# Kernel tuning notes

Hardware: AMD Instinct MI355X
Metric: run time of the kernel (lower is better)

## Reference

```python
import jax, jax.numpy as jnp
import numpy as np

N_HEAD = 16
HEAD_DIM = 64
N_EMBD = N_HEAD * HEAD_DIM  # 1024


def setup_inputs() -> dict:
    key = jax.random.key(0)
    ks = jax.random.split(key, 5)
    B, S = 2, 2048
    x = jax.random.normal(ks[0], (B, S, N_EMBD), dtype=jnp.float32)
    qkv_w = jax.random.normal(ks[1], (N_EMBD, 3 * N_EMBD), dtype=jnp.float32) * 0.02
    qkv_b = jax.random.normal(ks[2], (3 * N_EMBD,), dtype=jnp.float32) * 0.02
    proj_w = jax.random.normal(ks[3], (N_EMBD, N_EMBD), dtype=jnp.float32) * 0.02
    proj_b = jax.random.normal(ks[4], (N_EMBD,), dtype=jnp.float32) * 0.02
    return {"x": x, "qkv_w": qkv_w, "qkv_b": qkv_b, "proj_w": proj_w, "proj_b": proj_b}


def reference(x, qkv_w, qkv_b, proj_w, proj_b):
    B, S, _ = x.shape
    qkv = x @ qkv_w + qkv_b  # [B,S,3E]
    q, k, v = jnp.split(qkv, 3, axis=-1)
    # [B,H,S,D]
    q = q.reshape(B, S, N_HEAD, HEAD_DIM).transpose(0, 2, 1, 3)
    k = k.reshape(B, S, N_HEAD, HEAD_DIM).transpose(0, 2, 1, 3)
    v = v.reshape(B, S, N_HEAD, HEAD_DIM).transpose(0, 2, 1, 3)
    scale = 1.0 / jnp.sqrt(jnp.float32(HEAD_DIM))
    scores = jnp.einsum('bhqd,bhkd->bhqk', q, k) * scale  # [B,H,S,S]
    causal = jnp.tril(jnp.ones((S, S), dtype=bool))
    scores = jnp.where(causal[None, None], scores, jnp.float32(-jnp.inf))
    attn = jax.nn.softmax(scores, axis=-1)  # dropout p=0 (eval)
    out = jnp.einsum('bhqk,bhkd->bhqd', attn, v)
    out = out.transpose(0, 2, 1, 3).reshape(B, S, N_EMBD)
    out = out @ proj_w + proj_b  # resid dropout p=0
    return out, k, v
```

## Files before the change

### kernel.cpp

```cpp
#include <hip/hip_runtime.h>
#include <hip/hip_bf16.h>


typedef __attribute__((ext_vector_type(4))) float f32x4;
typedef __attribute__((ext_vector_type(16))) float f32x16;
typedef __attribute__((ext_vector_type(8))) short s16x8;
typedef __attribute__((ext_vector_type(4))) short s16x4;

__device__ __forceinline__ short f2bf(float f) {
    union { float f; unsigned u; } x{f};
    unsigned r = x.u + 0x7fff + ((x.u >> 16) & 1);
    return (short)(r >> 16);
}

__device__ __forceinline__ void gload_lds16(const void* g, void* l) {
    __builtin_amdgcn_global_load_lds(
        (const __attribute__((address_space(1))) void*)g,
        (__attribute__((address_space(3))) void*)l, 16, 0, 0);
}

__global__ __launch_bounds__(256) void fused_prepass(const float* __restrict__ x,
                                                     short* __restrict__ x_bf,
                                                     const float* __restrict__ qkv_w,
                                                     short* __restrict__ wT1,
                                                     const float* __restrict__ proj_w,
                                                     short* __restrict__ wT2) {
    __shared__ float tile[32][33];
    const int bid = blockIdx.x, tid = threadIdx.x;
    if (bid < 2048) {
        int i = (bid * 256 + tid) * 8;
        f32x4 a = *(const f32x4*)&x[i];
        f32x4 b = *(const f32x4*)&x[i + 4];
        s16x8 o;
        #pragma unroll
        for (int j = 0; j < 4; ++j) o[j] = f2bf(a[j]);
        #pragma unroll
        for (int j = 0; j < 4; ++j) o[j + 4] = f2bf(b[j]);
        *(s16x8*)&x_bf[i] = o;
        return;
    }
    const float* in;
    short* out;
    int K = 1024, N, n0, k0;
    if (bid < 5120) {
        int blk = bid - 2048;
        in = qkv_w; out = wT1; N = 3072;
        n0 = (blk % 96) * 32; k0 = (blk / 96) * 32;
    } else {
        int blk = bid - 5120;
        in = proj_w; out = wT2; N = 1024;
        n0 = (blk & 31) * 32; k0 = (blk >> 5) * 32;
    }
    const int tx = tid & 31, ty = tid >> 5;
    #pragma unroll
    for (int r = 0; r < 4; ++r)
        tile[ty + r * 8][tx] = in[(long)(k0 + ty + r * 8) * N + n0 + tx];
    __syncthreads();
    #pragma unroll
    for (int r = 0; r < 4; ++r)
        out[(long)(n0 + ty + r * 8) * K + k0 + tx] = f2bf(tile[tx][ty + r * 8]);
}


template <int MODE>
__global__ __launch_bounds__(256) void gemm_bf16(
    const short* __restrict__ A, const short* __restrict__ Bt,
    const float* __restrict__ bias, int M, int N, int K,
    float* __restrict__ outf,
    short* __restrict__ qbf, short* __restrict__ kbf, short* __restrict__ vbfT,
    float* __restrict__ kout, float* __restrict__ vout) {
    __shared__ __align__(16) short As[128 * 32];
    __shared__ __align__(16) short Bs[128 * 32];
    const int tid = threadIdx.x;
    const int l = tid & 63, w = tid >> 6;
    const int lr = l >> 4, lc = l & 15;
    const int wm = w >> 1, wn = w & 1;
    const int m0 = blockIdx.y * 128, n0 = blockIdx.x * 128;

    f32x4 acc[4][4] = {};
    const int c0 = tid, c1 = tid + 256;

    for (int kb = 0; kb < K; kb += 32) {
        __syncthreads();
        gload_lds16(A + (long)(m0 + (c0 >> 2)) * K + kb + (c0 & 3) * 8, As + c0 * 8);
        gload_lds16(A + (long)(m0 + (c1 >> 2)) * K + kb + (c1 & 3) * 8, As + c1 * 8);
        gload_lds16(Bt + (long)(n0 + (c0 >> 2)) * K + kb + (c0 & 3) * 8, Bs + c0 * 8);
        gload_lds16(Bt + (long)(n0 + (c1 >> 2)) * K + kb + (c1 & 3) * 8, Bs + c1 * 8);
        __syncthreads();
        s16x8 af[4], bfr[4];
        #pragma unroll
        for (int mi = 0; mi < 4; ++mi)
            af[mi] = *(const s16x8*)&As[(wm * 64 + mi * 16 + lc) * 32 + lr * 8];
        #pragma unroll
        for (int ni = 0; ni < 4; ++ni)
            bfr[ni] = *(const s16x8*)&Bs[(wn * 64 + ni * 16 + lc) * 32 + lr * 8];
        #pragma unroll
        for (int mi = 0; mi < 4; ++mi)
            #pragma unroll
            for (int ni = 0; ni < 4; ++ni)
                acc[mi][ni] = __builtin_amdgcn_mfma_f32_16x16x32_bf16(
                    af[mi], bfr[ni], acc[mi][ni], 0, 0, 0);
    }

    #pragma unroll
    for (int mi = 0; mi < 4; ++mi) {
        #pragma unroll
        for (int ni = 0; ni < 4; ++ni) {
            int col = n0 + wn * 64 + ni * 16 + lc;
            float bv = bias[col];
            if (MODE == 1) {
                int sec = col >> 10, rem = col & 1023;
                int h = rem >> 6, d = rem & 63;
                int row0 = m0 + wm * 64 + mi * 16 + lr * 4;
                int b = row0 >> 11, s0 = row0 & 2047;
                long idxSD = ((long)((b << 4) + h) * 2048 + s0) * 64 + d;
                if (sec == 0) {
                    #pragma unroll
                    for (int i = 0; i < 4; ++i) {
                        float val = acc[mi][ni][i] + bv;
                        qbf[idxSD + (long)i * 64] = f2bf(val * 0.1803368801111244f);
                    }
                } else if (sec == 1) {
                    #pragma unroll
                    for (int i = 0; i < 4; ++i) {
                        float val = acc[mi][ni][i] + bv;
                        kout[idxSD + (long)i * 64] = val;
                        kbf[idxSD + (long)i * 64] = f2bf(val);
                    }
                } else {
                    s16x4 pk;
                    #pragma unroll
                    for (int i = 0; i < 4; ++i) {
                        float val = acc[mi][ni][i] + bv;
                        vout[idxSD + (long)i * 64] = val;
                        pk[i] = f2bf(val);
                    }
                    *(s16x4*)&vbfT[((long)((b << 4) + h) * 64 + d) * 2048 + s0] = pk;
                }
            } else {
                #pragma unroll
                for (int i = 0; i < 4; ++i) {
                    int row = m0 + wm * 64 + mi * 16 + lr * 4 + i;
                    outf[(long)row * N + col] = acc[mi][ni][i] + bv;
                }
            }
        }
    }
}

__global__ __launch_bounds__(256, 2) void attn_kernel(const short* __restrict__ qbf,
                                                      const short* __restrict__ kbf,
                                                      const short* __restrict__ vbfT,
                                                      short* __restrict__ obf) {
    const int bid = blockIdx.x;
    const int xcd = bid & 7, r = bid >> 3;
    const int head_local = r & 3, q16 = r >> 2;
    const int qt = (q16 < 8) ? (q16 + 8) : (15 - q16);
    const int bh = xcd * 4 + head_local;
    const int tid = threadIdx.x;
    const int wv = tid >> 6, l = tid & 63;
    const int h = l >> 5;
    const int l8 = l & 7;
    const int q0 = qt * 128 + wv * 32;
    const int qlane = q0 + (l & 31);
    const long baseSD = (long)bh * 2048 * 64;
    const long baseDS = (long)bh * 64 * 2048;

    __shared__ __align__(16) short Ks[2][64 * 64];
    __shared__ __align__(16) short Vs[2][64 * 64];

    const int sSub = l >> 3;
    const int sChunk = (l & 7) ^ sSub;
    auto stage = [&](int kt, int nb) {
        const int k0 = kt * 64;
        const int r0 = wv * 16 + sSub;
        gload_lds16(kbf + baseSD + (long)(k0 + r0) * 64 + sChunk * 8,
                    &Ks[nb][(wv * 16) * 64]);
        gload_lds16(kbf + baseSD + (long)(k0 + r0 + 8) * 64 + sChunk * 8,
                    &Ks[nb][(wv * 16 + 8) * 64]);
        gload_lds16(vbfT + baseDS + (long)r0 * 2048 + k0 + sChunk * 8,
                    &Vs[nb][(wv * 16) * 64]);
        gload_lds16(vbfT + baseDS + (long)(r0 + 8) * 2048 + k0 + sChunk * 8,
                    &Vs[nb][(wv * 16 + 8) * 64]);
    };

    s16x8 qf[4];
    #pragma unroll
    for (int dd = 0; dd < 4; ++dd)
        qf[dd] = *(const s16x8*)&qbf[baseSD + (long)qlane * 64 + dd * 16 + h * 8];

    f32x4 lacc = {};
    f32x16 O[2] = {};

    const int nkt = 2 * qt + 2;

    stage(0, 0);
    __syncthreads();
    int cur = 0;

    for (int kt = 0; kt < nkt; ++kt) {
        const int k0 = kt * 64;
        if (kt + 1 < nkt) stage(kt + 1, cur ^ 1);

        if (k0 <= q0 + 31) {
            const short* Kb = Ks[cur];
            const short* Vb = Vs[cur];
            #pragma unroll
            for (int kk2 = 0; kk2 < 2; ++kk2) {
                f32x16 z = {};
                #pragma unroll
                for (int dd = 0; dd < 4; ++dd) {
                    s16x8 kf = *(const s16x8*)&Kb[(kk2 * 32 + (l & 31)) * 64 +
                                                  (((2 * dd + h) ^ l8) * 8)];
                    z = __builtin_amdgcn_mfma_f32_32x32x16_bf16(kf, qf[dd], z, 0, 0, 0);
                }
                if (k0 + 63 > q0) {
                    #pragma unroll
                    for (int rr = 0; rr < 16; ++rr) {
                        int kpos = k0 + kk2 * 32 + (rr & 3) + 8 * (rr >> 2) + 4 * h;
                        if (kpos > qlane) z[rr] = -INFINITY;
                    }
                }
                float p[16];
                #pragma unroll
                for (int rr = 0; rr < 16; ++rr) {
                    p[rr] = __builtin_amdgcn_exp2f(z[rr]);
                    lacc[rr & 3] += p[rr];
                }
                #pragma unroll
                for (int f = 0; f < 2; ++f) {
                    union { __hip_bfloat162 b2[4]; s16x8 v; } pk;
                    #pragma unroll
                    for (int j = 0; j < 4; ++j)
                        pk.b2[j] = __float22bfloat162_rn(
                            make_float2(p[f * 8 + 2 * j], p[f * 8 + 2 * j + 1]));
                    const int c0 = kk2 * 4 + f * 2;
                    #pragma unroll
                    for (int dt2 = 0; dt2 < 2; ++dt2) {
                        const short* vr = &Vb[(dt2 * 32 + (l & 31)) * 64];
                        s16x8 vf;
                        *(s16x4*)&vf = *(const s16x4*)&vr[(c0 ^ l8) * 8 + 4 * h];
                        *(((s16x4*)&vf) + 1) = *(const s16x4*)&vr[((c0 + 1) ^ l8) * 8 + 4 * h];
                        O[dt2] = __builtin_amdgcn_mfma_f32_32x32x16_bf16(vf, pk.v,
                                                                         O[dt2], 0, 0, 0);
                    }
                }
            }
        }
        __syncthreads();
        cur ^= 1;
    }

    float lsum = (lacc[0] + lacc[1]) + (lacc[2] + lacc[3]);
    lsum += __shfl_xor(lsum, 32);
    const int b = bh >> 4, hd = bh & 15;
    float inv = 1.0f / lsum;
    #pragma unroll
    for (int dt2 = 0; dt2 < 2; ++dt2) {
        #pragma unroll
        for (int g = 0; g < 4; ++g) {
            s16x4 o;
            #pragma unroll
            for (int i = 0; i < 4; ++i) o[i] = f2bf(O[dt2][g * 4 + i] * inv);
            const int d = dt2 * 32 + 8 * g + 4 * h;
            *(s16x4*)&obf[(long)(b * 2048 + qlane) * 1024 + hd * 64 + d] = o;
        }
    }
}


extern "C" void kernel_launch(void* const* d_in, const int* in_sizes, int n_in,
                              void* d_out, int out_size, void* d_ws, size_t ws_size,
                              hipStream_t stream) {
    const float* x = (const float*)d_in[0];
    const float* qkv_w = (const float*)d_in[1];
    const float* qkv_b = (const float*)d_in[2];
    const float* proj_w = (const float*)d_in[3];
    const float* proj_b = (const float*)d_in[4];

    float* out = (float*)d_out;
    float* kout = out + 4194304;
    float* vout = out + 8388608;

    short* x_bf = (short*)d_ws;
    short* wT1 = x_bf + 4194304;
    short* wT2 = wT1 + 3145728;
    short* q_bf = wT2 + 1048576;
    short* k_bf = q_bf + 4194304;
    short* vT_bf = k_bf + 4194304;
    short* o_bf = x_bf;

    fused_prepass<<<6144, 256, 0, stream>>>(x, x_bf, qkv_w, wT1, proj_w, wT2);

    gemm_bf16<1><<<dim3(24, 32), 256, 0, stream>>>(x_bf, wT1, qkv_b, 4096, 3072, 1024,
                                                   nullptr, q_bf, k_bf, vT_bf, kout, vout);

    attn_kernel<<<512, 256, 0, stream>>>(q_bf, k_bf, vT_bf, o_bf);

    gemm_bf16<2><<<dim3(8, 32), 256, 0, stream>>>(o_bf, wT2, proj_b, 4096, 1024, 1024,
                                                  out, nullptr, nullptr, nullptr, nullptr, nullptr);
}
```

Baseline: 121.3 us.

## Double GEMM K-tile, XOR-swizzle LDS, and remap blocks per XCD

The bf16 GEMM now stages a 64-wide K slice per iteration instead of 32, which halves the number of barrier pairs and load rounds. Rows are stored in LDS with an XOR swizzle on the 16-byte segment index to avoid bank conflicts on the fragment reads. The 2D grid becomes a 1D grid remapped so each XCD (bid & 7) gets a contiguous rectangle of output tiles, improving L2 reuse of A and B. LDS use doubles to 32 KB per block, which may reduce occupancy.

```diff
diff --git a/kernel.cpp b/kernel.cpp
--- a/kernel.cpp
+++ b/kernel.cpp
@@ -61,7 +61,6 @@
         out[(long)(n0 + ty + r * 8) * K + k0 + tx] = f2bf(tile[tx][ty + r * 8]);
 }
 
-
 template <int MODE>
 __global__ __launch_bounds__(256) void gemm_bf16(
     const short* __restrict__ A, const short* __restrict__ Bt,
@@ -69,37 +68,52 @@
     float* __restrict__ outf,
     short* __restrict__ qbf, short* __restrict__ kbf, short* __restrict__ vbfT,
     float* __restrict__ kout, float* __restrict__ vout) {
-    __shared__ __align__(16) short As[128 * 32];
-    __shared__ __align__(16) short Bs[128 * 32];
+    __shared__ __align__(16) short As[128 * 64];
+    __shared__ __align__(16) short Bs[128 * 64];
     const int tid = threadIdx.x;
     const int l = tid & 63, w = tid >> 6;
     const int lr = l >> 4, lc = l & 15;
     const int wm = w >> 1, wn = w & 1;
-    const int m0 = blockIdx.y * 128, n0 = blockIdx.x * 128;
+    const int bid = blockIdx.x;
+    const int xcd = bid & 7, s = bid >> 3;
+    int bx, by;
+    if (MODE == 1) { bx = (xcd & 1) * 12 + s % 12; by = (xcd >> 1) * 8 + s / 12; }
+    else           { bx = (xcd & 1) * 4 + (s & 3); by = (xcd >> 1) * 8 + (s >> 2); }
+    const int m0 = by * 128, n0 = bx * 128;
 
     f32x4 acc[4][4] = {};
-    const int c0 = tid, c1 = tid + 256;
-
-    for (int kb = 0; kb < K; kb += 32) {
+
+    for (int kb = 0; kb < K; kb += 64) {
         __syncthreads();
-        gload_lds16(A + (long)(m0 + (c0 >> 2)) * K + kb + (c0 & 3) * 8, As + c0 * 8);
-        gload_lds16(A + (long)(m0 + (c1 >> 2)) * K + kb + (c1 & 3) * 8, As + c1 * 8);
-        gload_lds16(Bt + (long)(n0 + (c0 >> 2)) * K + kb + (c0 & 3) * 8, Bs + c0 * 8);
-        gload_lds16(Bt + (long)(n0 + (c1 >> 2)) * K + kb + (c1 & 3) * 8, Bs + c1 * 8);
+        #pragma unroll
+        for (int j = 0; j < 4; ++j) {
+            const int c = tid + 256 * j;
+            const int row = c >> 3;
+            const int lseg = (c & 7) ^ (row & 7);
+            gload_lds16(A + (long)(m0 + row) * K + kb + lseg * 8, As + c * 8);
+            gload_lds16(Bt + (long)(n0 + row) * K + kb + lseg * 8, Bs + c * 8);
+        }
         __syncthreads();
-        s16x8 af[4], bfr[4];
-        #pragma unroll
-        for (int mi = 0; mi < 4; ++mi)
-            af[mi] = *(const s16x8*)&As[(wm * 64 + mi * 16 + lc) * 32 + lr * 8];
-        #pragma unroll
-        for (int ni = 0; ni < 4; ++ni)
-            bfr[ni] = *(const s16x8*)&Bs[(wn * 64 + ni * 16 + lc) * 32 + lr * 8];
-        #pragma unroll
-        for (int mi = 0; mi < 4; ++mi)
-            #pragma unroll
-            for (int ni = 0; ni < 4; ++ni)
-                acc[mi][ni] = __builtin_amdgcn_mfma_f32_16x16x32_bf16(
-                    af[mi], bfr[ni], acc[mi][ni], 0, 0, 0);
+        #pragma unroll
+        for (int kh = 0; kh < 2; ++kh) {
+            s16x8 af[4], bfr[4];
+            #pragma unroll
+            for (int mi = 0; mi < 4; ++mi) {
+                const int row = wm * 64 + mi * 16 + lc;
+                af[mi] = *(const s16x8*)&As[row * 64 + (((kh * 4 + lr) ^ (lc & 7)) * 8)];
+            }
+            #pragma unroll
+            for (int ni = 0; ni < 4; ++ni) {
+                const int row = wn * 64 + ni * 16 + lc;
+                bfr[ni] = *(const s16x8*)&Bs[row * 64 + (((kh * 4 + lr) ^ (lc & 7)) * 8)];
+            }
+            #pragma unroll
+            for (int mi = 0; mi < 4; ++mi)
+                #pragma unroll
+                for (int ni = 0; ni < 4; ++ni)
+                    acc[mi][ni] = __builtin_amdgcn_mfma_f32_16x16x32_bf16(
+                        af[mi], bfr[ni], acc[mi][ni], 0, 0, 0);
+        }
     }
 
     #pragma unroll
@@ -292,11 +306,11 @@
 
     fused_prepass<<<6144, 256, 0, stream>>>(x, x_bf, qkv_w, wT1, proj_w, wT2);
 
-    gemm_bf16<1><<<dim3(24, 32), 256, 0, stream>>>(x_bf, wT1, qkv_b, 4096, 3072, 1024,
-                                                   nullptr, q_bf, k_bf, vT_bf, kout, vout);
+    gemm_bf16<1><<<768, 256, 0, stream>>>(x_bf, wT1, qkv_b, 4096, 3072, 1024,
+                                          nullptr, q_bf, k_bf, vT_bf, kout, vout);
 
     attn_kernel<<<512, 256, 0, stream>>>(q_bf, k_bf, vT_bf, o_bf);
 
-    gemm_bf16<2><<<dim3(8, 32), 256, 0, stream>>>(o_bf, wT2, proj_b, 4096, 1024, 1024,
-                                                  out, nullptr, nullptr, nullptr, nullptr, nullptr);
-}
+    gemm_bf16<2><<<256, 256, 0, stream>>>(o_bf, wT2, proj_b, 4096, 1024, 1024,
+                                          out, nullptr, nullptr, nullptr, nullptr, nullptr);
+}
```

New measurement: 109.7 us. 1.11x faster.
